# Kernel optimization log

Hardware: AMD Instinct MI355X
Metric: run time of the kernel (lower is better)

The kernel has to match this reference:

```python
import jax, jax.numpy as jnp
import numpy as np

N = 128                      # reduced state dimension (Q_dim[0])
S = N * (N + 1) // 2         # number of triu pairwise products = 8256
BATCH = 16384                # snapshot columns
_rows, _cols = np.triu_indices(N)
ROWS = jnp.asarray(_rows)    # [S] int32 constants
COLS = jnp.asarray(_cols)


def setup_inputs() -> dict:
    key = jax.random.key(0)
    kx, ka, kb = jax.random.split(key, 3)
    x = jax.random.normal(kx, (N, BATCH), dtype=jnp.float32)
    # learned operators (module inits them to zeros; use small random for a meaningful baseline)
    A = jax.random.normal(ka, (N, N), dtype=jnp.float32) * 0.02
    B = jax.random.normal(kb, (N, S), dtype=jnp.float32) * 0.02
    return {"x": x, "A": A, "B": B}


def reference(x, A, B):
    # quadratic feature expansion: x2[k, :] = x[i_k, :] * x[j_k, :] over triu pairs
    x2 = x[ROWS] * x[COLS]                 # [S, BATCH]
    return A @ x + B @ x2                  # [N, BATCH]
```

## Files before the change

kernel.cpp:

```cpp
#include <hip/hip_runtime.h>


constexpr int N_     = 128;
constexpr int S_     = 8256;
constexpr int BATCH_ = 16384;
constexpr int KTOT   = 8384;
constexpr int NKT    = 131;
constexpr size_t WT_BYTES = (size_t)KTOT * 128 * 2;
constexpr size_t PP_OFF   = WT_BYTES;
constexpr size_t XH_OFF   = PP_OFF + 32768;

typedef __attribute__((ext_vector_type(8))) _Float16 half8;
typedef __attribute__((ext_vector_type(2))) _Float16 half2t;
typedef __attribute__((ext_vector_type(4))) float f32x4;

__device__ __forceinline__ ushort f2h(float f) {
    _Float16 h = (_Float16)f;
    ushort b; __builtin_memcpy(&b, &h, 2); return b;
}
__device__ __forceinline__ float h2f(ushort b) {
    _Float16 h; __builtin_memcpy(&h, &b, 2); return (float)h;
}
__device__ __forceinline__ half2t duph(ushort b) {
    uint w = ((uint)b << 16) | (uint)b;
    half2t d; __builtin_memcpy(&d, &w, 4); return d;
}
__device__ __forceinline__ half8 mul_bc(half8 w, half2t d) {
    union { half8 h; half2t p[4]; } u, r;
    u.h = w;
    #pragma unroll
    for (int q = 0; q < 4; ++q) r.p[q] = u.p[q] * d;
    return r.h;
}

__device__ __forceinline__ int cumN(int i) {
    if (i <= 0) return 0;
    const int n = i - 1, t = n >> 3, r = n & 7;
    return 16 * i - (4 * t * (t + 1) + r * (t + 1));
}
__device__ __forceinline__ int offR(int i) {
    const int a = i >> 3, b = i & 7;
    const int p = b ? (8 * (b - 1) - (((b - 1) * b) >> 1)) : 0;
    return 28 * a + p;
}
__device__ __forceinline__ int triS(int i) { return i * (257 - i) / 2; }

__global__ __launch_bounds__(256) void build_all(
    const float* __restrict__ x,
    const float* __restrict__ A, const float* __restrict__ B,
    ushort* __restrict__ pp, ushort* __restrict__ wt,
    ushort* __restrict__ xh)
{
    const int bid = blockIdx.x, t = threadIdx.x;
    if (bid < 524) {
        const int idx = bid * 256 + t;
        const int ko  = idx >> 7;
        const int m   = idx & 127;
        const int kt = ko >> 3, kk = (ko >> 2) & 1, oct = ko & 3;
        const int lane = oct * 16 + (m & 15);
        const int e0 = kt * 8192 + kk * 4096 + (m >> 6) * 2048 +
                       ((m >> 4) & 3) * 512 + lane * 8;
        float v[8];
        if (ko < 16) {
            const int i0 = ko * 8;
            #pragma unroll
            for (int el = 0; el < 8; ++el) v[el] = A[m * 128 + i0 + el];
        } else if (ko < 992) {
            const int o = ko - 16;
            int i = 0;
            #pragma unroll
            for (int st = 64; st >= 1; st >>= 1) {
                const int c = i + st;
                if (c < 128 && cumN(c) <= o) i = c;
            }
            const int jb = ((i + 7) >> 3) + (o - cumN(i));
            const int s0 = triS(i) + jb * 8 - i;
            const float* bp = B + (size_t)m * S_ + s0;
            #pragma unroll
            for (int el = 0; el < 8; ++el) v[el] = bp[el];
        } else {
            const int kb = ko * 8 - 7936;
            #pragma unroll
            for (int el = 0; el < 8; ++el) {
                const int kloc = kb + el;
                int i = 0;
                #pragma unroll
                for (int st = 64; st >= 1; st >>= 1) {
                    const int c = i + st;
                    if (c < 128 && offR(c) <= kloc) i = c;
                }
                v[el] = B[(size_t)m * S_ + triS(i) + (kloc - offR(i))];
            }
        }
        ushort o8[8];
        #pragma unroll
        for (int el = 0; el < 8; ++el) o8[el] = f2h(v[el]);
        __builtin_memcpy(wt + e0, o8, 16);
    } else if (bid == 524) {
        const int i = t;
        if (i < 128) {
            pp[i] = (ushort)(i | (0xFFu << 8));
            const int jb0 = (i + 7) >> 3;
            int kb = 128 + cumN(i) * 8;
            for (int jb = jb0; jb < 16; ++jb) {
                #pragma unroll
                for (int e = 0; e < 8; ++e)
                    pp[kb + e] = (ushort)(i | ((jb * 8 + e) << 8));
                kb += 8;
            }
            const int h = (8 - (i & 7)) & 7;
            const int rb = 7936 + offR(i);
            for (int e = 0; e < h; ++e)
                pp[rb + e] = (ushort)(i | ((i + e) << 8));
        }
    } else {
        const int col = (bid - 525) * 256 + t;
        ushort* xc = xh + (size_t)col * 128;
        const int cs = col & 15;
        #pragma unroll
        for (int ro = 0; ro < 16; ++ro) {
            uint ow[4];
            #pragma unroll
            for (int p = 0; p < 4; ++p) {
                const ushort u0 = f2h(x[(size_t)(ro * 8 + 2 * p) * BATCH_ + col]);
                const ushort u1 = f2h(x[(size_t)(ro * 8 + 2 * p + 1) * BATCH_ + col]);
                ow[p] = (uint)u0 | ((uint)u1 << 16);
            }
            __builtin_memcpy(xc + ((ro ^ cs) << 3), ow, 16);
        }
    }
}

__device__ __forceinline__ void load_af4(half8 af[4], const ushort* __restrict__ wt,
                                         int kt, int mb, int wm, int lane) {
    const ushort* ab = wt + ((size_t)kt << 13) + (mb << 11) + (wm << 10) +
                       (lane << 3);
    #pragma unroll
    for (int kk = 0; kk < 2; ++kk)
        #pragma unroll
        for (int mt = 0; mt < 2; ++mt)
            af[kk * 2 + mt] = *(const half8*)(ab + (kk << 12) + (mt << 9));
}

__global__ __launch_bounds__(256) void gemm_mfma(
    const ushort* __restrict__ xh,
    const ushort* __restrict__ wt,
    const ushort* __restrict__ pp,
    float* __restrict__ out)
{
    __shared__ ushort xt[64 * 128];
    __shared__ uint   ppc[NKT * 4];

    const int t    = threadIdx.x;
    const int b0   = blockIdx.x * 64;
    const int mb   = blockIdx.y;
    const int lane = t & 63;
    const int w    = t >> 6;
    const int wm   = w >> 1, wn = w & 1;
    const int l16  = lane & 15, quad = lane >> 4;
    const int sw   = l16 << 3;

    {
        const ushort* src = xh + (size_t)b0 * 128;
        #pragma unroll
        for (int i = 0; i < 4; ++i)
            *(half8*)(xt + i * 2048 + t * 8) =
                *(const half8*)(src + i * 2048 + t * 8);
    }
    for (int idx = t; idx < NKT * 4; idx += 256) {
        const int kt = idx >> 2, q = idx & 3;
        const uint a0 = *(const uint*)(pp + kt * 64 + q * 8);
        const uint a1 = *(const uint*)(pp + kt * 64 + 32 + q * 8);
        ppc[idx] = (a0 & 0xFFFFu) | ((a1 & 0xFFFFu) << 16);
    }
    __syncthreads();

    f32x4 acc[2][2];
    #pragma unroll
    for (int mt = 0; mt < 2; ++mt)
        #pragma unroll
        for (int nt = 0; nt < 2; ++nt)
            acc[mt][nt] = (f32x4){0.f, 0.f, 0.f, 0.f};

    const ushort* xbase = xt + (wn * 32 + l16) * 128;

    for (int kt = 0; kt < 2; ++kt) {
        half8 af[4];
        load_af4(af, wt, kt, mb, wm, lane);
        #pragma unroll
        for (int kk = 0; kk < 2; ++kk) {
            const int off = (kt * 64 + kk * 32 + quad * 8) ^ sw;
            #pragma unroll
            for (int nt = 0; nt < 2; ++nt) {
                const half8 bfr = *(const half8*)(xbase + nt * 2048 + off);
                #pragma unroll
                for (int mt = 0; mt < 2; ++mt)
                    acc[mt][nt] = __builtin_amdgcn_mfma_f32_16x16x32_f16(
                        af[kk * 2 + mt], bfr, acc[mt][nt], 0, 0, 0);
            }
        }
    }

    for (int kt = 2; kt < 124; ++kt) {
        half8 af[4];
        load_af4(af, wt, kt, mb, wm, lane);
        const uint prc = ppc[kt * 4 + quad];
        const int ia = (int)(prc & 0xFFu) ^ sw;
        const int ja = (int)((prc >> 8) & 0xFFu) ^ sw;
        const int ib = (int)((prc >> 16) & 0xFFu) ^ sw;
        const int jb = (int)(prc >> 24) ^ sw;

        ushort xi[2][2]; half8 wj[2][2];
        #pragma unroll
        for (int nt = 0; nt < 2; ++nt) {
            const ushort* xb = xbase + nt * 2048;
            xi[0][nt] = xb[ia];
            xi[1][nt] = xb[ib];
            wj[0][nt] = *(const half8*)(xb + ja);
            wj[1][nt] = *(const half8*)(xb + jb);
        }

        half8 bfr[2][2];
        #pragma unroll
        for (int kk = 0; kk < 2; ++kk)
            #pragma unroll
            for (int nt = 0; nt < 2; ++nt)
                bfr[kk][nt] = mul_bc(wj[kk][nt], duph(xi[kk][nt]));

        __builtin_amdgcn_s_setprio(1);
        #pragma unroll
        for (int kk = 0; kk < 2; ++kk)
            #pragma unroll
            for (int nt = 0; nt < 2; ++nt)
                #pragma unroll
                for (int mt = 0; mt < 2; ++mt)
                    acc[mt][nt] = __builtin_amdgcn_mfma_f32_16x16x32_f16(
                        af[kk * 2 + mt], bfr[kk][nt], acc[mt][nt], 0, 0, 0);
        __builtin_amdgcn_s_setprio(0);
    }

    for (int kt = 124; kt < NKT; ++kt) {
        half8 af[4];
        load_af4(af, wt, kt, mb, wm, lane);
        #pragma unroll
        for (int kk = 0; kk < 2; ++kk) {
            const int k0 = kt * 64 + kk * 32 + quad * 8;
            const uint4 pk = *(const uint4*)(pp + k0);
            const uint pr4[4] = {pk.x, pk.y, pk.z, pk.w};
            #pragma unroll
            for (int nt = 0; nt < 2; ++nt) {
                const ushort* xb = xbase + nt * 2048;
                float prods[8];
                #pragma unroll
                for (int e = 0; e < 8; ++e) {
                    const uint ent = (pr4[e >> 1] >> ((e & 1) * 16)) & 0xFFFFu;
                    prods[e] = h2f(xb[(int)(ent & 0xFFu) ^ sw]) *
                               h2f(xb[(int)(ent >> 8) ^ sw]);
                }
                union { half8 h; uint wdw[4]; } bb;
                #pragma unroll
                for (int p = 0; p < 4; ++p) {
                    const auto pk2 = __builtin_amdgcn_cvt_pkrtz(
                        prods[2 * p], prods[2 * p + 1]);
                    __builtin_memcpy(&bb.wdw[p], &pk2, 4);
                }
                const half8 bfr = bb.h;
                #pragma unroll
                for (int mt = 0; mt < 2; ++mt)
                    acc[mt][nt] = __builtin_amdgcn_mfma_f32_16x16x32_f16(
                        af[kk * 2 + mt], bfr, acc[mt][nt], 0, 0, 0);
            }
        }
    }

    #pragma unroll
    for (int mt = 0; mt < 2; ++mt) {
        #pragma unroll
        for (int nt = 0; nt < 2; ++nt) {
            const int mbase = mb * 64 + wm * 32 + mt * 16 + quad * 4;
            const size_t col = (size_t)b0 + wn * 32 + nt * 16 + l16;
            #pragma unroll
            for (int r = 0; r < 4; ++r)
                out[(size_t)(mbase + r) * BATCH_ + col] = acc[mt][nt][r];
        }
    }
}

extern "C" void kernel_launch(void* const* d_in, const int* in_sizes, int n_in,
                              void* d_out, int out_size, void* d_ws, size_t ws_size,
                              hipStream_t stream) {
    const float* x = (const float*)d_in[0];
    const float* A = (const float*)d_in[1];
    const float* B = (const float*)d_in[2];
    float* out = (float*)d_out;

    ushort* wt = (ushort*)d_ws;
    ushort* pp = (ushort*)((char*)d_ws + PP_OFF);
    ushort* xh = (ushort*)((char*)d_ws + XH_OFF);

    build_all<<<589, 256, 0, stream>>>(x, A, B, pp, wt, xh);
    gemm_mfma<<<dim3(BATCH_ / 64, 2), 256, 0, stream>>>(xh, wt, pp, out);
}
```

Measured before the change: 130.8 us.

## Split K across four blocks with atomic accumulation and widen tile to 128 columns

Result: no change. 129.2 us (-1.3%).

```diff
diff --git a/kernel.cpp b/kernel.cpp
--- a/kernel.cpp
+++ b/kernel.cpp
@@ -49,7 +49,7 @@
     const float* __restrict__ x,
     const float* __restrict__ A, const float* __restrict__ B,
     ushort* __restrict__ pp, ushort* __restrict__ wt,
-    ushort* __restrict__ xh)
+    ushort* __restrict__ xh, float* __restrict__ out)
 {
     const int bid = blockIdx.x, t = threadIdx.x;
     if (bid < 524) {
@@ -96,7 +96,13 @@
         #pragma unroll
         for (int el = 0; el < 8; ++el) o8[el] = f2h(v[el]);
         __builtin_memcpy(wt + e0, o8, 16);
-    } else if (bid == 524) {
+    } else if (bid < 780) {
+        const int zb = bid - 524;
+        f32x4* o4 = (f32x4*)out;
+        #pragma unroll
+        for (int c = 0; c < 4; ++c)
+            o4[(size_t)zb * 2048 + c * 512 + t] = (f32x4){0.f, 0.f, 0.f, 0.f};
+    } else if (bid == 780) {
         const int i = t;
         if (i < 128) {
             pp[i] = (ushort)(i | (0xFFu << 8));
@@ -114,7 +120,7 @@
                 pp[rb + e] = (ushort)(i | ((i + e) << 8));
         }
     } else {
-        const int col = (bid - 525) * 256 + t;
+        const int col = (bid - 781) * 256 + t;
         ushort* xc = xh + (size_t)col * 128;
         const int cs = col & 15;
         #pragma unroll
@@ -131,15 +137,14 @@
     }
 }
 
-__device__ __forceinline__ void load_af4(half8 af[4], const ushort* __restrict__ wt,
-                                         int kt, int mb, int wm, int lane) {
-    const ushort* ab = wt + ((size_t)kt << 13) + (mb << 11) + (wm << 10) +
-                       (lane << 3);
+__device__ __forceinline__ void load_af8(half8 af[8], const ushort* __restrict__ wt,
+                                         int kt, int mb, int lane) {
+    const ushort* ab = wt + ((size_t)kt << 13) + (mb << 11) + (lane << 3);
     #pragma unroll
     for (int kk = 0; kk < 2; ++kk)
         #pragma unroll
-        for (int mt = 0; mt < 2; ++mt)
-            af[kk * 2 + mt] = *(const half8*)(ab + (kk << 12) + (mt << 9));
+        for (int mt = 0; mt < 4; ++mt)
+            af[kk * 4 + mt] = *(const half8*)(ab + (kk << 12) + (mt << 9));
 }
 
 __global__ __launch_bounds__(256) void gemm_mfma(
@@ -148,22 +153,27 @@
     const ushort* __restrict__ pp,
     float* __restrict__ out)
 {
-    __shared__ ushort xt[64 * 128];
+    __shared__ ushort xt[128 * 128];
     __shared__ uint   ppc[NKT * 4];
 
     const int t    = threadIdx.x;
-    const int b0   = blockIdx.x * 64;
-    const int mb   = blockIdx.y;
+    const int b0   = blockIdx.x * 128;
+    const int mb   = blockIdx.y & 1;
+    const int sp   = blockIdx.y >> 1;
+    const int kt0  = sp * 33;
+    const int kt1  = (sp == 3) ? NKT : kt0 + 33;
     const int lane = t & 63;
-    const int w    = t >> 6;
-    const int wm   = w >> 1, wn = w & 1;
+    const int wn   = t >> 6;
     const int l16  = lane & 15, quad = lane >> 4;
     const int sw   = l16 << 3;
 
+    const int s_ni = (kt0 > 2) ? kt0 : 2;
+    const int e_ni = (kt1 < 124) ? kt1 : 124;
+
     {
         const ushort* src = xh + (size_t)b0 * 128;
         #pragma unroll
-        for (int i = 0; i < 4; ++i)
+        for (int i = 0; i < 8; ++i)
             *(half8*)(xt + i * 2048 + t * 8) =
                 *(const half8*)(src + i * 2048 + t * 8);
     }
@@ -175,35 +185,37 @@
     }
     __syncthreads();
 
-    f32x4 acc[2][2];
+    f32x4 acc[4][2];
     #pragma unroll
-    for (int mt = 0; mt < 2; ++mt)
+    for (int mt = 0; mt < 4; ++mt)
         #pragma unroll
         for (int nt = 0; nt < 2; ++nt)
             acc[mt][nt] = (f32x4){0.f, 0.f, 0.f, 0.f};
 
     const ushort* xbase = xt + (wn * 32 + l16) * 128;
 
-    for (int kt = 0; kt < 2; ++kt) {
-        half8 af[4];
-        load_af4(af, wt, kt, mb, wm, lane);
-        #pragma unroll
-        for (int kk = 0; kk < 2; ++kk) {
-            const int off = (kt * 64 + kk * 32 + quad * 8) ^ sw;
-            #pragma unroll
-            for (int nt = 0; nt < 2; ++nt) {
-                const half8 bfr = *(const half8*)(xbase + nt * 2048 + off);
-                #pragma unroll
-                for (int mt = 0; mt < 2; ++mt)
-                    acc[mt][nt] = __builtin_amdgcn_mfma_f32_16x16x32_f16(
-                        af[kk * 2 + mt], bfr, acc[mt][nt], 0, 0, 0);
-            }
-        }
-    }
-
-    for (int kt = 2; kt < 124; ++kt) {
-        half8 af[4];
-        load_af4(af, wt, kt, mb, wm, lane);
+    if (sp == 0) {
+        for (int kt = 0; kt < 2; ++kt) {
+            half8 af[8];
+            load_af8(af, wt, kt, mb, lane);
+            #pragma unroll
+            for (int kk = 0; kk < 2; ++kk) {
+                const int off = (kt * 64 + kk * 32 + quad * 8) ^ sw;
+                #pragma unroll
+                for (int nt = 0; nt < 2; ++nt) {
+                    const half8 bfr = *(const half8*)(xbase + nt * 2048 + off);
+                    #pragma unroll
+                    for (int mt = 0; mt < 4; ++mt)
+                        acc[mt][nt] = __builtin_amdgcn_mfma_f32_16x16x32_f16(
+                            af[kk * 4 + mt], bfr, acc[mt][nt], 0, 0, 0);
+                }
+            }
+        }
+    }
+
+    for (int kt = s_ni; kt < e_ni; ++kt) {
+        half8 af[8];
+        load_af8(af, wt, kt, mb, lane);
         const uint prc = ppc[kt * 4 + quad];
         const int ia = (int)(prc & 0xFFu) ^ sw;
         const int ja = (int)((prc >> 8) & 0xFFu) ^ sw;
@@ -233,55 +245,58 @@
             #pragma unroll
             for (int nt = 0; nt < 2; ++nt)
                 #pragma unroll
-                for (int mt = 0; mt < 2; ++mt)
+                for (int mt = 0; mt < 4; ++mt)
                     acc[mt][nt] = __builtin_amdgcn_mfma_f32_16x16x32_f16(
-                        af[kk * 2 + mt], bfr[kk][nt], acc[mt][nt], 0, 0, 0);
+                        af[kk * 4 + mt], bfr[kk][nt], acc[mt][nt], 0, 0, 0);
         __builtin_amdgcn_s_setprio(0);
     }
 
-    for (int kt = 124; kt < NKT; ++kt) {
-        half8 af[4];
-        load_af4(af, wt, kt, mb, wm, lane);
-        #pragma unroll
-        for (int kk = 0; kk < 2; ++kk) {
-            const int k0 = kt * 64 + kk * 32 + quad * 8;
-            const uint4 pk = *(const uint4*)(pp + k0);
-            const uint pr4[4] = {pk.x, pk.y, pk.z, pk.w};
-            #pragma unroll
-            for (int nt = 0; nt < 2; ++nt) {
-                const ushort* xb = xbase + nt * 2048;
-                float prods[8];
-                #pragma unroll
-                for (int e = 0; e < 8; ++e) {
-                    const uint ent = (pr4[e >> 1] >> ((e & 1) * 16)) & 0xFFFFu;
-                    prods[e] = h2f(xb[(int)(ent & 0xFFu) ^ sw]) *
-                               h2f(xb[(int)(ent >> 8) ^ sw]);
+    if (sp == 3) {
+        for (int kt = 124; kt < NKT; ++kt) {
+            half8 af[8];
+            load_af8(af, wt, kt, mb, lane);
+            #pragma unroll
+            for (int kk = 0; kk < 2; ++kk) {
+                const int k0 = kt * 64 + kk * 32 + quad * 8;
+                const uint4 pk = *(const uint4*)(pp + k0);
+                const uint pr4[4] = {pk.x, pk.y, pk.z, pk.w};
+                #pragma unroll
+                for (int nt = 0; nt < 2; ++nt) {
+                    const ushort* xb = xbase + nt * 2048;
+                    float prods[8];
+                    #pragma unroll
+                    for (int e = 0; e < 8; ++e) {
+                        const uint ent = (pr4[e >> 1] >> ((e & 1) * 16)) & 0xFFFFu;
+                        prods[e] = h2f(xb[(int)(ent & 0xFFu) ^ sw]) *
+                                   h2f(xb[(int)(ent >> 8) ^ sw]);
+                    }
+                    union { half8 h; uint wdw[4]; } bb;
+                    #pragma unroll
+                    for (int p = 0; p < 4; ++p) {
+                        const auto pk2 = __builtin_amdgcn_cvt_pkrtz(
+                            prods[2 * p], prods[2 * p + 1]);
+                        __builtin_memcpy(&bb.wdw[p], &pk2, 4);
+                    }
+                    const half8 bfr = bb.h;
+                    #pragma unroll
+                    for (int mt = 0; mt < 4; ++mt)
+                        acc[mt][nt] = __builtin_amdgcn_mfma_f32_16x16x32_f16(
+                            af[kk * 4 + mt], bfr, acc[mt][nt], 0, 0, 0);
                 }
-                union { half8 h; uint wdw[4]; } bb;
-                #pragma unroll
-                for (int p = 0; p < 4; ++p) {
-                    const auto pk2 = __builtin_amdgcn_cvt_pkrtz(
-                        prods[2 * p], prods[2 * p + 1]);
-                    __builtin_memcpy(&bb.wdw[p], &pk2, 4);
-                }
-                const half8 bfr = bb.h;
-                #pragma unroll
-                for (int mt = 0; mt < 2; ++mt)
-                    acc[mt][nt] = __builtin_amdgcn_mfma_f32_16x16x32_f16(
-                        af[kk * 2 + mt], bfr, acc[mt][nt], 0, 0, 0);
             }
         }
     }
 
     #pragma unroll
-    for (int mt = 0; mt < 2; ++mt) {
+    for (int mt = 0; mt < 4; ++mt) {
         #pragma unroll
         for (int nt = 0; nt < 2; ++nt) {
-            const int mbase = mb * 64 + wm * 32 + mt * 16 + quad * 4;
+            const int mbase = mb * 64 + mt * 16 + quad * 4;
             const size_t col = (size_t)b0 + wn * 32 + nt * 16 + l16;
             #pragma unroll
             for (int r = 0; r < 4; ++r)
-                out[(size_t)(mbase + r) * BATCH_ + col] = acc[mt][nt][r];
+                unsafeAtomicAdd(&out[(size_t)(mbase + r) * BATCH_ + col],
+                                acc[mt][nt][r]);
         }
     }
 }
@@ -298,6 +313,6 @@
     ushort* pp = (ushort*)((char*)d_ws + PP_OFF);
     ushort* xh = (ushort*)((char*)d_ws + XH_OFF);
 
-    build_all<<<589, 256, 0, stream>>>(x, A, B, pp, wt, xh);
-    gemm_mfma<<<dim3(BATCH_ / 64, 2), 256, 0, stream>>>(xh, wt, pp, out);
-}
+    build_all<<<845, 256, 0, stream>>>(x, A, B, pp, wt, xh, out);
+    gemm_mfma<<<dim3(BATCH_ / 128, 8), 256, 0, stream>>>(xh, wt, pp, out);
+}
```
